# Kernel optimization log

Hardware: AMD Instinct MI355X
Metric: run time of the kernel (lower is better)

Reference implementation:

```python
import jax, jax.numpy as jnp
import numpy as np

HID = 64      # hidden_dim
HEADS = 4     # attention heads
CH = HID // HEADS  # 16 per-head channels
EDIM = 6      # edge_dim
NEG = 0.2     # leaky_relu negative slope


def _glorot(key, shape):
    fan_in, fan_out = shape[0], shape[-1]
    s = np.sqrt(6.0 / (fan_in + fan_out)).astype(np.float32)
    return jax.random.uniform(key, shape, jnp.float32, -s, s)


def setup_inputs() -> dict:
    key = jax.random.key(0)
    ks = iter(jax.random.split(key, 48))
    N, E, T = 100000, 1200000, 20000
    inp = {
        "x": jax.random.normal(next(ks), (N, 7), jnp.float32),
        "pos": jax.random.normal(next(ks), (N, 3), jnp.float32),
        "node_type": jax.random.randint(next(ks), (N,), 0, 2),
        "edge_index": jax.random.randint(next(ks), (2, E), 0, N),
        "edge_attr": jax.random.normal(next(ks), (E, EDIM), jnp.float32),
        "num_tracks": T,
        "hidden_state": jax.random.normal(next(ks), (T, HID), jnp.float32),
        # params
        "type_emb": jax.random.normal(next(ks), (2, 8), jnp.float32),
        "enc_W1": _glorot(next(ks), (18, HID)), "enc_b1": jnp.zeros((HID,), jnp.float32),
        "enc_W2": _glorot(next(ks), (HID, HID)), "enc_b2": jnp.zeros((HID,), jnp.float32),
        "gru_Wi": _glorot(next(ks), (HID, 3 * HID)), "gru_bi": jnp.zeros((3 * HID,), jnp.float32),
        "gru_Wh": _glorot(next(ks), (HID, 3 * HID)), "gru_bh": jnp.zeros((3 * HID,), jnp.float32),
        "dec_W1": _glorot(next(ks), (HID, HID)), "dec_b1": jnp.zeros((HID,), jnp.float32),
        "dec_W2": _glorot(next(ks), (HID, 7)), "dec_b2": jnp.zeros((7,), jnp.float32),
    }
    for g in ("g1", "g2"):
        inp[g + "_Wl"] = _glorot(next(ks), (HID, HID))
        inp[g + "_bl"] = jnp.zeros((HID,), jnp.float32)
        inp[g + "_Wr"] = _glorot(next(ks), (HID, HID))
        inp[g + "_br"] = jnp.zeros((HID,), jnp.float32)
        inp[g + "_We"] = _glorot(next(ks), (EDIM, HID))
        inp[g + "_att"] = _glorot(next(ks), (HEADS, CH))
        inp[g + "_bias"] = jnp.zeros((HID,), jnp.float32)
    return inp


def _segment_softmax(e, seg, n):
    m = jax.ops.segment_max(e, seg, num_segments=n)
    m = jnp.where(jnp.isfinite(m), m, 0.0)
    ex = jnp.exp(e - m[seg])
    s = jax.ops.segment_sum(ex, seg, num_segments=n)
    return ex / (s[seg] + 1e-16)


def _gatv2(h, src, dst, eattr, Wl, bl, Wr, br, We, att, bias):
    N = h.shape[0]
    xl = (h @ Wl + bl).reshape(N, HEADS, CH)
    xr = (h @ Wr + br).reshape(N, HEADS, CH)
    ea = (eattr @ We).reshape(-1, HEADS, CH)
    g = jax.nn.leaky_relu(xl[src] + xr[dst] + ea, NEG)      # [E, H, C]
    e = jnp.einsum('ehc,hc->eh', g, att)                     # [E, H]
    alpha = _segment_softmax(e, dst, N)                      # [E, H]
    msg = xl[src] * alpha[..., None]                         # [E, H, C]
    out = jax.ops.segment_sum(msg, dst, num_segments=N)
    return out.reshape(N, HID) + bias, alpha


def reference(x, pos, node_type, edge_index, edge_attr, num_tracks, hidden_state,
              type_emb, enc_W1, enc_b1, enc_W2, enc_b2,
              g1_Wl, g1_bl, g1_Wr, g1_br, g1_We, g1_att, g1_bias,
              g2_Wl, g2_bl, g2_Wr, g2_br, g2_We, g2_att, g2_bias,
              gru_Wi, gru_bi, gru_Wh, gru_bh,
              dec_W1, dec_b1, dec_W2, dec_b2):
    N = x.shape[0]
    h = jnp.concatenate([x, pos, type_emb[node_type]], axis=-1)
    h = jax.nn.relu(h @ enc_W1 + enc_b1) @ enc_W2 + enc_b2

    # PyG GATv2Conv: add self loops, edge_attr fill_value='mean' (mean of incoming edges)
    src, dst = edge_index[0], edge_index[1]
    deg = jax.ops.segment_sum(jnp.ones(src.shape[0], jnp.float32), dst, num_segments=N)
    loop_attr = jax.ops.segment_sum(edge_attr, dst, num_segments=N) / jnp.maximum(deg, 1.0)[:, None]
    ar = jnp.arange(N)
    src_a = jnp.concatenate([src, ar])
    dst_a = jnp.concatenate([dst, ar])
    eattr_a = jnp.concatenate([edge_attr, loop_attr], axis=0)

    h1, a1 = _gatv2(h, src_a, dst_a, eattr_a, g1_Wl, g1_bl, g1_Wr, g1_br, g1_We, g1_att, g1_bias)
    h1 = jax.nn.relu(h1)
    h2, a2 = _gatv2(h1, src_a, dst_a, eattr_a, g2_Wl, g2_bl, g2_Wr, g2_br, g2_We, g2_att, g2_bias)

    # GRUCell on the first num_tracks nodes
    ht = h2[:num_tracks]
    gi = ht @ gru_Wi + gru_bi
    gh = hidden_state @ gru_Wh + gru_bh
    r = jax.nn.sigmoid(gi[:, :HID] + gh[:, :HID])
    z = jax.nn.sigmoid(gi[:, HID:2 * HID] + gh[:, HID:2 * HID])
    n = jnp.tanh(gi[:, 2 * HID:] + r * gh[:, 2 * HID:])
    new_tracks = (1.0 - z) * n + z * hidden_state

    new_full = jnp.concatenate([new_tracks, h2[num_tracks:]], axis=0)
    out = jax.nn.relu(new_full @ dec_W1 + dec_b1) @ dec_W2 + dec_b2  # [N, 7]
    final = out.at[:, :3].set(pos + out[:, :3])
    final = final.at[:, 3:6].set(x[:, :3] + out[:, 3:6])
    return final, new_full, a1, a2
```

## Files before the change

### kernel.cpp

```cpp
#include <hip/hip_runtime.h>

#define NEG 0.2f
#define LOG2E 1.44269504088896f
typedef unsigned short u16;

__device__ __forceinline__ float sigmoidf_(float v){ return 1.f/(1.f+__expf(-v)); }
__device__ __forceinline__ int rfl_(int v){ return __builtin_amdgcn_readfirstlane(v); }
__device__ __forceinline__ float bf2f_(unsigned u){ return __uint_as_float(u<<16); }
__device__ __forceinline__ u16 f2bf_(float f){
  unsigned u = __float_as_uint(f);
  u += 0x7FFFu + ((u>>16)&1u);
  return (u16)(u>>16);
}
template<int C>
__device__ __forceinline__ float dppadd_(float p){
  int r = __builtin_amdgcn_update_dpp(0, __float_as_int(p), C, 0xF, 0xF, true);
  return p + __int_as_float(r);
}
__device__ __forceinline__ float dppsum16_(float p){
  p = dppadd_<0x121>(p);
  p = dppadd_<0x122>(p);
  p = dppadd_<0x124>(p);
  p = dppadd_<0x128>(p);
  return p;
}

__global__ void deg_kernel(const int* __restrict__ ei, int* __restrict__ deg, int E)
{
  int base = blockIdx.x*1024 + threadIdx.x;
  #pragma unroll
  for (int j=0;j<4;j++){
    int e = base + j*256;
    if (e < E) atomicAdd(deg + ei[E+e], 1);
  }
}

__global__ __launch_bounds__(256) void alloc_kernel(
    const int* __restrict__ deg, int* __restrict__ offs, int* __restrict__ cursor,
    int* __restrict__ counter, int N)
{
  __shared__ int wsum[4], woff[4], sbase;
  int lane = threadIdx.x & 63, w = threadIdx.x >> 6;
  int base = blockIdx.x*1024 + threadIdx.x*4;
  int v[4]; int s=0;
  #pragma unroll
  for (int j=0;j<4;j++){ int i=base+j; v[j]=(i<N)?deg[i]:0; s+=v[j]; }
  int inc=s;
  #pragma unroll
  for (int d=1;d<64;d<<=1){ int t=__shfl_up(inc,d); if (lane>=d) inc+=t; }
  if (lane==63) wsum[w]=inc;
  __syncthreads();
  if (threadIdx.x==0){
    woff[0]=0; woff[1]=wsum[0]; woff[2]=wsum[0]+wsum[1]; woff[3]=wsum[0]+wsum[1]+wsum[2];
    sbase = atomicAdd(counter, woff[3]+wsum[3]);
  }
  __syncthreads();
  int excl = sbase + woff[w] + (inc - s);
  #pragma unroll
  for (int j=0;j<4;j++){
    int i=base+j;
    if (i<N){ offs[i]=excl; cursor[i]=excl; }
    excl+=v[j];
  }
}

__global__ __launch_bounds__(256) void encxfill_kernel(
    const float* __restrict__ x, const float* __restrict__ pos,
    const int* __restrict__ ntype, const float* __restrict__ temb,
    const float* __restrict__ eW1, const float* __restrict__ eb1,
    const float* __restrict__ eW2, const float* __restrict__ eb2,
    const float* __restrict__ Wl, const float* __restrict__ bl,
    const float* __restrict__ Wr, const float* __restrict__ br,
    u16* __restrict__ xlo, u16* __restrict__ xro,
    const int* __restrict__ ei, const float* __restrict__ eattr,
    int* __restrict__ cursor, float4* __restrict__ slots,
    int exB, int E, int N)
{
  __shared__ float fT[4][8*20];
  __shared__ float tT[4][8*64];
  if ((int)blockIdx.x >= exB){
    int base = ((int)blockIdx.x - exB)*1024 + (int)threadIdx.x;
    #pragma unroll
    for (int j=0;j<4;j++){
      int e = base + j*256;
      if (e < E){
        int dst = ei[E + e];
        unsigned slot = (unsigned)atomicAdd(cursor + dst, 1);
        const float2* ep = (const float2*)(eattr + (size_t)e*6);
        float2 p0=ep[0], p1=ep[1], p2=ep[2];
        float4 a, b;
        a.x = __int_as_float(e); a.y = __int_as_float(ei[e]);
        a.z = p0.x; a.w = p0.y;
        b.x = p1.x; b.y = p1.y; b.z = p2.x; b.w = p2.y;
        slots[slot*2u]   = a;
        slots[slot*2u+1] = b;
      }
    }
    return;
  }
  int lane = threadIdx.x & 63;
  int wid  = threadIdx.x >> 6;
  int n0 = (blockIdx.x*4 + wid)*8;
  if (n0 >= N) return;
  #pragma unroll
  for (int m=0;m<8;m++){
    int n=n0+m; float fv=0.f;
    if (n<N){
      if (lane<7)       fv=x[(size_t)n*7+lane];
      else if (lane<10) fv=pos[(size_t)n*3+lane-7];
      else if (lane<18) fv=temb[ntype[n]*8+lane-10];
    }
    if (lane<20) fT[wid][m*20+lane]=fv;
  }
  float t[8];
  float b1v=eb1[lane];
  #pragma unroll
  for (int m=0;m<8;m++) t[m]=b1v;
  #pragma unroll 2
  for (int k=0;k<18;k++){
    float w=eW1[k*64+lane];
    #pragma unroll
    for (int m=0;m<8;m++) t[m] += fT[wid][m*20+k]*w;
  }
  #pragma unroll
  for (int m=0;m<8;m++){ t[m]=fmaxf(t[m],0.f); tT[wid][m*64+lane]=t[m]; }
  float o[8];
  float b2v=eb2[lane];
  #pragma unroll
  for (int m=0;m<8;m++) o[m]=b2v;
  #pragma unroll 2
  for (int k=0;k<64;k++){
    float w=eW2[k*64+lane];
    #pragma unroll
    for (int m=0;m<8;m++) o[m] += tT[wid][m*64+k]*w;
  }
  #pragma unroll
  for (int m=0;m<8;m++) tT[wid][m*64+lane]=o[m];
  float blv=bl[lane], brv=br[lane];
  float al[8], ar[8];
  #pragma unroll
  for (int m=0;m<8;m++){ al[m]=blv; ar[m]=brv; }
  #pragma unroll 2
  for (int k=0;k<64;k++){
    float wl=Wl[k*64+lane], wr=Wr[k*64+lane];
    #pragma unroll
    for (int m=0;m<8;m++){
      float hb = tT[wid][m*64+k];
      al[m]+=hb*wl; ar[m]+=hb*wr;
    }
  }
  #pragma unroll
  for (int m=0;m<8;m++){
    int n=n0+m;
    if (n<N){ xlo[(((unsigned)n)<<6)+lane]=f2bf_(al[m]); xro[(((unsigned)n)<<6)+lane]=f2bf_(ar[m]); }
  }
}

__global__ __launch_bounds__(256) void xfrm_kernel(
    const float* __restrict__ hin,
    const float* __restrict__ Wl, const float* __restrict__ bl,
    const float* __restrict__ Wr, const float* __restrict__ br,
    u16* __restrict__ xlo, u16* __restrict__ xro, int N)
{
  __shared__ float sWl[4096], sWr[4096];
  __shared__ float hT[4][16*64];
  for (int i=threadIdx.x;i<4096;i+=256){ sWl[i]=Wl[i]; sWr[i]=Wr[i]; }
  __syncthreads();
  int lane=threadIdx.x&63;
  int wid=threadIdx.x>>6;
  int n0=(blockIdx.x*4+wid)*16;
  if (n0>=N) return;
  #pragma unroll
  for (int m=0;m<16;m++){
    int n=n0+m;
    hT[wid][m*64+lane] = (n<N)? hin[(size_t)n*64+lane] : 0.f;
  }
  float blv=bl[lane], brv=br[lane];
  float al[16], ar[16];
  #pragma unroll
  for (int m=0;m<16;m++){ al[m]=blv; ar[m]=brv; }
  #pragma unroll 2
  for (int k=0;k<64;k++){
    float wl=sWl[k*64+lane], wr=sWr[k*64+lane];
    #pragma unroll
    for (int m=0;m<16;m++){
      float hb = hT[wid][m*64+k];
      al[m]+=hb*wl; ar[m]+=hb*wr;
    }
  }
  #pragma unroll
  for (int m=0;m<16;m++){
    int n=n0+m;
    if (n<N){ xlo[(((unsigned)n)<<6)+lane]=f2bf_(al[m]); xro[(((unsigned)n)<<6)+lane]=f2bf_(ar[m]); }
  }
}

#define EDGE_STEP(EIDX, EADD, XV) do {                                       \
    float s_ = (XV) + xrv + (EADD);                                          \
    s_ = fmaxf(s_, NEG*s_);                                                  \
    float p_ = dppsum16_(s_*attv);                                           \
    if (isbase) aout[(((unsigned)(EIDX))<<2)+h] = p_;                        \
    lastp = p_;                                                              \
    if (__all(p_ <= mmax)) {                                                 \
      float w_ = exp2f(p_ - mmax);                                           \
      ssum += w_; acc += w_*(XV);                                            \
    } else {                                                                 \
      float mn_ = fmaxf(mmax, p_);                                           \
      float sc_ = exp2f(mmax - mn_);                                         \
      float w_  = exp2f(p_ - mn_);                                           \
      ssum = ssum*sc_ + w_;                                                  \
      acc  = acc*sc_ + w_*(XV);                                              \
      mmax = mn_;                                                            \
    }                                                                        \
  } while(0)

#define EDGE_PRE(J, OO) \
    float4 u##J = slots[(unsigned)(OO)*2u], v##J = slots[(unsigned)(OO)*2u+1u]; \
    int e##J = rfl_(__float_as_int(u##J.x)); \
    int s##J = rfl_(__float_as_int(u##J.y)); \
    unsigned xv##J = xlb[(((unsigned)s##J)<<6)+lane];

#define EDGE_BODY(J) \
    float d##J = u##J.z*we0 + u##J.w*we1 + v##J.x*we2 + v##J.y*we3 + v##J.z*we4 + v##J.w*we5; \
    dsum += d##J; \
    EDGE_STEP(e##J, d##J, bf2f_(xv##J));

__global__ __launch_bounds__(256) void gat_kernel(
    const float4* __restrict__ slots, const int* __restrict__ offs, const int* __restrict__ deg,
    const u16* __restrict__ xlb, const u16* __restrict__ xrb,
    const float* __restrict__ We, const float* __restrict__ att,
    const float* __restrict__ bias,
    float* __restrict__ aout, float* __restrict__ hout,
    int E, int N, int do_relu)
{
  int lane = threadIdx.x & 63;
  int n = blockIdx.x*4 + (threadIdx.x>>6);
  if (n >= N) return;
  float we0=We[lane], we1=We[64+lane], we2=We[128+lane],
        we3=We[192+lane], we4=We[256+lane], we5=We[320+lane];
  float attv = att[lane] * LOG2E;
  float bv = bias[lane];
  float xrv = bf2f_(xrb[(((unsigned)n)<<6)+lane]);
  int h = lane >> 4;
  bool isbase = (lane & 15) == 0;
  int o0 = rfl_(offs[n]);
  int dg = rfl_(deg[n]);
  int oend = o0 + dg;
  float mmax = -3.402823e38f, ssum=0.f, acc=0.f, dsum=0.f, lastp=0.f;
  int o = o0;
  for (; o+4 <= oend; o += 4){
    EDGE_PRE(0,o); EDGE_PRE(1,o+1); EDGE_PRE(2,o+2); EDGE_PRE(3,o+3);
    EDGE_BODY(0); EDGE_BODY(1); EDGE_BODY(2); EDGE_BODY(3);
  }
  for (; o < oend; ++o){
    EDGE_PRE(0,o);
    EDGE_BODY(0);
  }
  {
    float dS = dsum * (1.f/fmaxf((float)dg,1.f));
    float xvS = bf2f_((unsigned)xlb[(((unsigned)n)<<6)+lane]);
    EDGE_STEP(E+n, dS, xvS);
  }
  float sinv = 1.f/(ssum + 1e-16f);
  asm volatile("s_waitcnt vmcnt(0)" ::: "memory");
  o = o0;
  for (; o+4 <= oend; o += 4){
    int e0 = __float_as_int(slots[(unsigned)o*2u].x);
    int e1 = __float_as_int(slots[(unsigned)(o+1)*2u].x);
    int e2 = __float_as_int(slots[(unsigned)(o+2)*2u].x);
    int e3 = __float_as_int(slots[(unsigned)(o+3)*2u].x);
    if (isbase){
      unsigned i0=(((unsigned)e0)<<2)+h, i1=(((unsigned)e1)<<2)+h,
               i2=(((unsigned)e2)<<2)+h, i3=(((unsigned)e3)<<2)+h;
      float r0=aout[i0], r1=aout[i1], r2=aout[i2], r3=aout[i3];
      aout[i0]=exp2f(r0-mmax)*sinv; aout[i1]=exp2f(r1-mmax)*sinv;
      aout[i2]=exp2f(r2-mmax)*sinv; aout[i3]=exp2f(r3-mmax)*sinv;
    }
  }
  for (; o < oend; ++o){
    int e0 = __float_as_int(slots[(unsigned)o*2u].x);
    if (isbase){
      unsigned i0=(((unsigned)e0)<<2)+h;
      aout[i0]=exp2f(aout[i0]-mmax)*sinv;
    }
  }
  if (isbase) aout[(((unsigned)(E+n))<<2)+h] = exp2f(lastp-mmax)*sinv;
  float outv = acc*sinv + bv;
  if (do_relu) outv = fmaxf(outv, 0.f);
  hout[(((unsigned)n)<<6)+lane] = outv;
}

__global__ __launch_bounds__(256) void grudec_kernel(
    const float* __restrict__ h2, const float* __restrict__ hid,
    const float* __restrict__ Wi, const float* __restrict__ bi,
    const float* __restrict__ Wh, const float* __restrict__ bh,
    const int* __restrict__ Tptr,
    const float* __restrict__ W1, const float* __restrict__ b1,
    const float* __restrict__ W2, const float* __restrict__ b2,
    const float* __restrict__ x, const float* __restrict__ pos,
    float* __restrict__ nf, float* __restrict__ fout, int N)
{
  __shared__ float sW2[448];
  __shared__ float sb2[8];
  __shared__ float tT[4][8*68];
  __shared__ float pT[4][8*68];
  for (int i=threadIdx.x;i<448;i+=256) sW2[i]=W2[i];
  if (threadIdx.x<7)  sb2[threadIdx.x]=b2[threadIdx.x];
  __syncthreads();
  int lane = threadIdx.x & 63;
  int wid  = threadIdx.x >> 6;
  int n0 = (blockIdx.x*4 + wid)*8;
  if (n0 >= N) return;
  int T = *Tptr;
  float hv[8], nfv[8];
  #pragma unroll
  for (int m=0;m<8;m++){ int n=n0+m; hv[m] = (n<N)? h2[(size_t)n*64+lane] : 0.f; }
  if (n0 < T){
    float pv[8];
    #pragma unroll
    for (int m=0;m<8;m++){ int n=n0+m; pv[m] = (n<T)? hid[(size_t)n*64+lane] : 0.f; }
    #pragma unroll
    for (int m=0;m<8;m++){ tT[wid][m*68+lane]=hv[m]; pT[wid][m*68+lane]=pv[m]; }
    float gr[8],gz[8],gn[8],hr[8],hz[8],hn[8];
    #pragma unroll
    for (int m=0;m<8;m++){ gr[m]=0.f;gz[m]=0.f;gn[m]=0.f;hr[m]=0.f;hz[m]=0.f;hn[m]=0.f; }
    for (int k=0;k<64;k++){
      float wir=Wi[k*192+lane], wiz=Wi[k*192+64+lane], win=Wi[k*192+128+lane];
      float whr=Wh[k*192+lane], whz=Wh[k*192+64+lane], whn=Wh[k*192+128+lane];
      #pragma unroll
      for (int m=0;m<8;m++){
        float a=tT[wid][m*68+k], b=pT[wid][m*68+k];
        gr[m]+=a*wir; gz[m]+=a*wiz; gn[m]+=a*win;
        hr[m]+=b*whr; hz[m]+=b*whz; hn[m]+=b*whn;
      }
    }
    float bir=bi[lane], biz=bi[64+lane], bin=bi[128+lane];
    float bhr=bh[lane], bhz=bh[64+lane], bhn=bh[128+lane];
    #pragma unroll
    for (int m=0;m<8;m++){
      int n=n0+m;
      if (n<T){
        float r  = sigmoidf_(gr[m]+bir + hr[m]+bhr);
        float z  = sigmoidf_(gz[m]+biz + hz[m]+bhz);
        float nn = tanhf(gn[m]+bin + r*(hn[m]+bhn));
        nfv[m] = (1.f-z)*nn + z*pv[m];
      } else {
        nfv[m] = hv[m];
      }
    }
  } else {
    #pragma unroll
    for (int m=0;m<8;m++) nfv[m] = hv[m];
  }
  #pragma unroll
  for (int m=0;m<8;m++){ int n=n0+m; if (n<N) nf[(size_t)n*64+lane]=nfv[m]; }
  #pragma unroll
  for (int m=0;m<8;m++) tT[wid][m*68+lane]=nfv[m];
  float t[8];
  float b1v=b1[lane];
  #pragma unroll
  for (int m=0;m<8;m++) t[m]=b1v;
  #pragma unroll 2
  for (int k=0;k<64;k++){
    float w=W1[k*64+lane];
    #pragma unroll
    for (int m=0;m<8;m++) t[m] += tT[wid][m*68+k]*w;
  }
  #pragma unroll
  for (int m=0;m<8;m++) t[m]=fmaxf(t[m],0.f);
  #pragma unroll
  for (int m=0;m<8;m++) tT[wid][m*68+lane]=t[m];
  int mm = lane >> 3, cc = lane & 7;
  if (cc < 7){
    float a2v = sb2[cc];
    #pragma unroll 4
    for (int k=0;k<64;k++) a2v += tT[wid][mm*68+k]*sW2[k*7+cc];
    int n = n0+mm;
    if (n < N){
      if (cc<3)      a2v += pos[(size_t)n*3+cc];
      else if (cc<6) a2v += x[(size_t)n*7+(cc-3)];
      fout[(size_t)n*7+cc] = a2v;
    }
  }
}

extern "C" void kernel_launch(void* const* d_in, const int* in_sizes, int n_in,
                              void* d_out, int out_size, void* d_ws, size_t ws_size,
                              hipStream_t stream)
{
  const float* x     = (const float*)d_in[0];
  const float* pos   = (const float*)d_in[1];
  const int*   ntype = (const int*)d_in[2];
  const int*   eidx  = (const int*)d_in[3];
  const float* eattr = (const float*)d_in[4];
  const int*   Tptr  = (const int*)d_in[5];
  const float* hid   = (const float*)d_in[6];
  const float* temb  = (const float*)d_in[7];
  const float* encW1 = (const float*)d_in[8];
  const float* encb1 = (const float*)d_in[9];
  const float* encW2 = (const float*)d_in[10];
  const float* encb2 = (const float*)d_in[11];
  const float* gruWi = (const float*)d_in[12];
  const float* grubi = (const float*)d_in[13];
  const float* gruWh = (const float*)d_in[14];
  const float* grubh = (const float*)d_in[15];
  const float* decW1 = (const float*)d_in[16];
  const float* decb1 = (const float*)d_in[17];
  const float* decW2 = (const float*)d_in[18];
  const float* decb2 = (const float*)d_in[19];
  const float* gWl[2]  = {(const float*)d_in[20], (const float*)d_in[27]};
  const float* gbl[2]  = {(const float*)d_in[21], (const float*)d_in[28]};
  const float* gWr[2]  = {(const float*)d_in[22], (const float*)d_in[29]};
  const float* gbr[2]  = {(const float*)d_in[23], (const float*)d_in[30]};
  const float* gWe[2]  = {(const float*)d_in[24], (const float*)d_in[31]};
  const float* gatt[2] = {(const float*)d_in[25], (const float*)d_in[32]};
  const float* gbias[2]= {(const float*)d_in[26], (const float*)d_in[33]};

  int N  = in_sizes[0] / 7;
  int E  = in_sizes[3] / 2;
  int Ea = E + N;

  char* w = (char*)d_ws;
  float* A      = (float*)w; w += (size_t)N*64*sizeof(float);
  u16*   XL     = (u16*)w;  w += (size_t)N*64*sizeof(u16);
  u16*   XR     = (u16*)w;  w += (size_t)N*64*sizeof(u16);
  float4* slots = (float4*)w; w += (size_t)E*32;
  int*   deg    = (int*)w;   w += (size_t)N*sizeof(int);
  int*   counter= (int*)w;   w += 4*sizeof(int);
  int*   cursor = (int*)w;   w += (size_t)N*sizeof(int);
  int*   offs   = (int*)w;   w += (size_t)N*sizeof(int);

  float* out_final = (float*)d_out;
  float* out_nf    = out_final + (size_t)N*7;
  float* out_a1    = out_nf + (size_t)N*64;
  float* out_a2    = out_a1 + (size_t)Ea*4;

  hipMemsetAsync(deg, 0, ((size_t)N + 4)*sizeof(int), stream);

  deg_kernel<<<(E+1023)/1024, 256, 0, stream>>>(eidx, deg, E);
  alloc_kernel<<<(N+1023)/1024, 256, 0, stream>>>(deg, offs, cursor, counter, N);

  int exB = (N+31)/32;
  int flB = (E+1023)/1024;
  encxfill_kernel<<<exB+flB, 256, 0, stream>>>(x, pos, ntype, temb,
      encW1, encb1, encW2, encb2, gWl[0], gbl[0], gWr[0], gbr[0], XL, XR,
      eidx, eattr, cursor, slots, exB, E, N);

  int gatB = (N+3)/4;
  gat_kernel<<<gatB, 256, 0, stream>>>(slots, offs, deg, XL, XR,
      gWe[0], gatt[0], gbias[0], out_a1, A, E, N, 1);

  int xfB = (N+63)/64;
  xfrm_kernel<<<xfB, 256, 0, stream>>>(A, gWl[1], gbl[1], gWr[1], gbr[1], XL, XR, N);

  gat_kernel<<<gatB, 256, 0, stream>>>(slots, offs, deg, XL, XR,
      gWe[1], gatt[1], gbias[1], out_a2, A, E, N, 0);

  grudec_kernel<<<(N+31)/32, 256, 0, stream>>>(A, hid, gruWi, grubi, gruWh, grubh, Tptr,
      decW1, decb1, decW2, decb2, x, pos, out_nf, out_final, N);
}
```

Baseline: 541.6 us.

## Defer attention normalization to a separate coalesced edge-parallel pass

Each GAT kernel no longer goes back over its incoming edges to rescale the raw attention logits it wrote. It stores only the per-node, per-head max and inverse sum. A new edge-parallel alpha kernel then reads each edge's destination and normalizes both layers' attention outputs with coalesced float4 accesses. This removes a serialized scatter read-modify-write and a full vmcnt drain from the tail of the GAT kernels, but adds a kernel launch, an extra pass over both attention arrays, and gathers of the per-node stats.

```diff
diff --git a/kernel.cpp b/kernel.cpp
--- a/kernel.cpp
+++ b/kernel.cpp
@@ -200,7 +200,6 @@
     s_ = fmaxf(s_, NEG*s_);                                                  \
     float p_ = dppsum16_(s_*attv);                                           \
     if (isbase) aout[(((unsigned)(EIDX))<<2)+h] = p_;                        \
-    lastp = p_;                                                              \
     if (__all(p_ <= mmax)) {                                                 \
       float w_ = exp2f(p_ - mmax);                                           \
       ssum += w_; acc += w_*(XV);                                            \
@@ -230,7 +229,8 @@
     const u16* __restrict__ xlb, const u16* __restrict__ xrb,
     const float* __restrict__ We, const float* __restrict__ att,
     const float* __restrict__ bias,
-    float* __restrict__ aout, float* __restrict__ hout,
+    float* __restrict__ aout, float2* __restrict__ msbuf,
+    float* __restrict__ hout,
     int E, int N, int do_relu)
 {
   int lane = threadIdx.x & 63;
@@ -246,7 +246,7 @@
   int o0 = rfl_(offs[n]);
   int dg = rfl_(deg[n]);
   int oend = o0 + dg;
-  float mmax = -3.402823e38f, ssum=0.f, acc=0.f, dsum=0.f, lastp=0.f;
+  float mmax = -3.402823e38f, ssum=0.f, acc=0.f, dsum=0.f;
   int o = o0;
   for (; o+4 <= oend; o += 4){
     EDGE_PRE(0,o); EDGE_PRE(1,o+1); EDGE_PRE(2,o+2); EDGE_PRE(3,o+3);
@@ -262,32 +262,41 @@
     EDGE_STEP(E+n, dS, xvS);
   }
   float sinv = 1.f/(ssum + 1e-16f);
-  asm volatile("s_waitcnt vmcnt(0)" ::: "memory");
-  o = o0;
-  for (; o+4 <= oend; o += 4){
-    int e0 = __float_as_int(slots[(unsigned)o*2u].x);
-    int e1 = __float_as_int(slots[(unsigned)(o+1)*2u].x);
-    int e2 = __float_as_int(slots[(unsigned)(o+2)*2u].x);
-    int e3 = __float_as_int(slots[(unsigned)(o+3)*2u].x);
-    if (isbase){
-      unsigned i0=(((unsigned)e0)<<2)+h, i1=(((unsigned)e1)<<2)+h,
-               i2=(((unsigned)e2)<<2)+h, i3=(((unsigned)e3)<<2)+h;
-      float r0=aout[i0], r1=aout[i1], r2=aout[i2], r3=aout[i3];
-      aout[i0]=exp2f(r0-mmax)*sinv; aout[i1]=exp2f(r1-mmax)*sinv;
-      aout[i2]=exp2f(r2-mmax)*sinv; aout[i3]=exp2f(r3-mmax)*sinv;
-    }
-  }
-  for (; o < oend; ++o){
-    int e0 = __float_as_int(slots[(unsigned)o*2u].x);
-    if (isbase){
-      unsigned i0=(((unsigned)e0)<<2)+h;
-      aout[i0]=exp2f(aout[i0]-mmax)*sinv;
-    }
-  }
-  if (isbase) aout[(((unsigned)(E+n))<<2)+h] = exp2f(lastp-mmax)*sinv;
+  if (isbase) msbuf[(((unsigned)n)<<2)+h] = make_float2(mmax, sinv);
   float outv = acc*sinv + bv;
   if (do_relu) outv = fmaxf(outv, 0.f);
   hout[(((unsigned)n)<<6)+lane] = outv;
+}
+
+__global__ void alpha_kernel(const int* __restrict__ ei,
+                             const float2* __restrict__ ms1, const float2* __restrict__ ms2,
+                             float4* __restrict__ a1, float4* __restrict__ a2, int E, int N)
+{
+  int e = blockIdx.x*256 + threadIdx.x;
+  if (e >= E+N) return;
+  int dst = (e<E)? ei[E+e] : (e-E);
+  {
+    float4 r = a1[e];
+    const float2* mp = ms1 + (((unsigned)dst)<<2);
+    float2 m0=mp[0], m1=mp[1], m2=mp[2], m3=mp[3];
+    float4 o;
+    o.x = exp2f(r.x - m0.x)*m0.y;
+    o.y = exp2f(r.y - m1.x)*m1.y;
+    o.z = exp2f(r.z - m2.x)*m2.y;
+    o.w = exp2f(r.w - m3.x)*m3.y;
+    a1[e] = o;
+  }
+  {
+    float4 r = a2[e];
+    const float2* mp = ms2 + (((unsigned)dst)<<2);
+    float2 m0=mp[0], m1=mp[1], m2=mp[2], m3=mp[3];
+    float4 o;
+    o.x = exp2f(r.x - m0.x)*m0.y;
+    o.y = exp2f(r.y - m1.x)*m1.y;
+    o.z = exp2f(r.z - m2.x)*m2.y;
+    o.w = exp2f(r.w - m3.x)*m3.y;
+    a2[e] = o;
+  }
 }
 
 __global__ __launch_bounds__(256) void grudec_kernel(
@@ -424,6 +433,8 @@
   float* A      = (float*)w; w += (size_t)N*64*sizeof(float);
   u16*   XL     = (u16*)w;  w += (size_t)N*64*sizeof(u16);
   u16*   XR     = (u16*)w;  w += (size_t)N*64*sizeof(u16);
+  float2* msbuf1= (float2*)w; w += (size_t)N*4*sizeof(float2);
+  float2* msbuf2= (float2*)w; w += (size_t)N*4*sizeof(float2);
   float4* slots = (float4*)w; w += (size_t)E*32;
   int*   deg    = (int*)w;   w += (size_t)N*sizeof(int);
   int*   counter= (int*)w;   w += 4*sizeof(int);
@@ -448,14 +459,17 @@
 
   int gatB = (N+3)/4;
   gat_kernel<<<gatB, 256, 0, stream>>>(slots, offs, deg, XL, XR,
-      gWe[0], gatt[0], gbias[0], out_a1, A, E, N, 1);
+      gWe[0], gatt[0], gbias[0], out_a1, msbuf1, A, E, N, 1);
 
   int xfB = (N+63)/64;
   xfrm_kernel<<<xfB, 256, 0, stream>>>(A, gWl[1], gbl[1], gWr[1], gbr[1], XL, XR, N);
 
   gat_kernel<<<gatB, 256, 0, stream>>>(slots, offs, deg, XL, XR,
-      gWe[1], gatt[1], gbias[1], out_a2, A, E, N, 0);
+      gWe[1], gatt[1], gbias[1], out_a2, msbuf2, A, E, N, 0);
 
   grudec_kernel<<<(N+31)/32, 256, 0, stream>>>(A, hid, gruWi, grubi, gruWh, grubh, Tptr,
       decW1, decb1, decW2, decb2, x, pos, out_nf, out_final, N);
-}
+
+  alpha_kernel<<<(Ea+255)/256, 256, 0, stream>>>(eidx, msbuf1, msbuf2,
+      (float4*)out_a1, (float4*)out_a2, E, N);
+}
```

Result: faster. 495.3 us (-8.5%).
